# Kernel tuning notes

Measured on AMD Instinct MI355X. Metric: run time of the kernel, lower is better.

The kernel has to match this reference:

```python
import math
import jax, jax.numpy as jnp
import numpy as np

MODEL_DIM = 4096
NUM_EXPERTS = 64
NUM_TOKENS = 8192
CAPACITY_FACTOR = 1.0


def setup_inputs() -> dict:
    key = jax.random.key(0)
    kx, kw = jax.random.split(key)
    x = jax.random.normal(kx, (NUM_TOKENS, MODEL_DIM), dtype=jnp.float32)
    # nn.Linear weight: [num_experts, model_dim]
    W = jax.random.normal(kw, (NUM_EXPERTS, MODEL_DIM), dtype=jnp.float32) * (1.0 / math.sqrt(MODEL_DIM))
    return {"x": x, "W": W}


def reference(x, W):
    # gating projection (no bias), cast to fp32 as in top1gating
    logits = jnp.matmul(x, W.T).astype(jnp.float32)  # [S, E]
    num_tokens, num_experts = logits.shape
    capacity = int(CAPACITY_FACTOR * math.ceil(num_tokens / num_experts))

    indices1_s = jnp.argmax(logits, axis=1)                        # [S]
    gates = jax.nn.softmax(logits, axis=1)                         # [S, E]
    mask1 = jax.nn.one_hot(indices1_s, num_experts, dtype=jnp.float32)  # [S, E]
    gates1_s = jnp.sum(gates * mask1, axis=1)                      # [S]
    # per-expert running position of each routed token
    locations1 = jnp.cumsum(mask1, axis=0) - 1.0                   # [S, E]
    locations1_s = jnp.sum(locations1 * mask1, axis=1)             # [S]

    return (indices1_s.astype(jnp.int32),
            capacity,
            locations1_s.astype(jnp.int32),
            gates1_s,
            num_experts)
```

## Files before the change

kernel.cpp:

```cpp
#include <hip/hip_runtime.h>
#include <math.h>

#define NTOK 8192
#define MDIM 4096
#define NEXP 64
#define CAPACITY 128.0f

#define OFF_IDX  0
#define OFF_CAP  8192
#define OFF_LOC  8193
#define OFF_GATE 16385
#define OFF_NE   24577

#define NSLICE 16
#define KSL    (MDIM / NSLICE)
#define KC     32
#define NCH    (KSL / KC)

#define WS_CNT_OFF  0
#define WS_RK_OFF   16384
#define WS_PART_OFF 24576

using bf16x8 = __attribute__((ext_vector_type(8))) short;
using f32x4  = __attribute__((ext_vector_type(4))) float;
typedef unsigned int u32;

static __device__ __forceinline__ u32 cvtpk(float a0, float a1) {
    u32 r;
    asm("v_cvt_pk_bf16_f32 %0, %1, %2" : "=v"(r) : "v"(a0), "v"(a1));
    return r;
}

static __device__ __forceinline__ void split2(
    float a0, float a1, u32& p1, u32& p2, u32& p3)
{
    p1 = cvtpk(a0, a1);
    float t0 = a0 - __uint_as_float(p1 << 16);
    float t1 = a1 - __uint_as_float(p1 & 0xffff0000u);
    p2 = cvtpk(t0, t1);
    float u0 = t0 - __uint_as_float(p2 << 16);
    float u1 = t1 - __uint_as_float(p2 & 0xffff0000u);
    p3 = cvtpk(u0, u1);
}

__global__ __launch_bounds__(512, 4) void gate_mfma(
    const float* __restrict__ x,
    const float* __restrict__ W,
    float* __restrict__ part)
{
    __shared__ __align__(16) unsigned short wl[12][64][32];

    const int tid   = threadIdx.x;
    const int lane  = tid & 63;
    const int wv    = tid >> 6;
    const int m     = lane & 15;
    const int g     = lane >> 4;
    const int tok0  = blockIdx.x * 256 + wv * 32;
    const int slice = blockIdx.y;
    const int k0    = slice * KSL;

    const float* __restrict__ xp = x + (size_t)(tok0 + m) * MDIM + k0 + g * 8;

    auto loadx = [&](int c, float4* d) {
        const float* p = xp + c * KC;
        d[0] = *(const float4*)(p);
        d[1] = *(const float4*)(p + 4);
        d[2] = *(const float4*)(p + 16 * MDIM);
        d[3] = *(const float4*)(p + 16 * MDIM + 4);
    };

    auto splitW = [&](int h) {
        #pragma unroll
        for (int r = 0; r < 4; ++r) {
            const int j4  = r * 512 + tid;
            const int e   = j4 >> 5;
            const int kk4 = j4 & 31;
            float4 v = *(const float4*)(W + (size_t)e * MDIM + k0 + h * 128 + kk4 * 4);
            const int c4     = kk4 >> 3;
            const int slog   = (kk4 >> 1) & 3;
            const int half16 = kk4 & 1;
            const int phys   = slog ^ ((e >> 1) & 3);
            u32 w1a, w2a, w3a, w1b, w2b, w3b;
            split2(v.x, v.y, w1a, w2a, w3a);
            split2(v.z, v.w, w1b, w2b, w3b);
            *(uint2*)&wl[c4 * 3 + 0][e][phys * 8 + half16 * 4] = make_uint2(w1a, w1b);
            *(uint2*)&wl[c4 * 3 + 1][e][phys * 8 + half16 * 4] = make_uint2(w2a, w2b);
            *(uint2*)&wl[c4 * 3 + 2][e][phys * 8 + half16 * 4] = make_uint2(w3a, w3b);
        }
    };

    auto cvt = [&](float4 lo, float4 hi, bf16x8& r0, bf16x8& r1, bf16x8& r2) {
        union { u32 u[4]; bf16x8 v; } P1, P2, P3;
        split2(lo.x, lo.y, P1.u[0], P2.u[0], P3.u[0]);
        split2(lo.z, lo.w, P1.u[1], P2.u[1], P3.u[1]);
        split2(hi.x, hi.y, P1.u[2], P2.u[2], P3.u[2]);
        split2(hi.z, hi.w, P1.u[3], P2.u[3], P3.u[3]);
        r0 = P1.v; r1 = P2.v; r2 = P3.v;
    };

    f32x4 acc[2][4];
    #pragma unroll
    for (int gr = 0; gr < 2; ++gr)
        #pragma unroll
        for (int nt = 0; nt < 4; ++nt) acc[gr][nt] = (f32x4){0.f, 0.f, 0.f, 0.f};

    float4 bufA[4], bufB[4];
    loadx(0, bufA);
    loadx(1, bufB);

    #pragma unroll
    for (int h = 0; h < 2; ++h) {
        if (h) __syncthreads();
        splitW(h);
        __syncthreads();

        #pragma unroll
        for (int c4 = 0; c4 < 4; ++c4) {
            const int c = h * 4 + c4;
            float4* buf = (c & 1) ? bufB : bufA;

            bf16x8 w[3][4];
            #pragma unroll
            for (int t = 0; t < 3; ++t)
                #pragma unroll
                for (int nt = 0; nt < 4; ++nt) {
                    const int e    = nt * 16 + m;
                    const int phys = g ^ ((e >> 1) & 3);
                    w[t][nt] = *(const bf16x8*)&wl[c4 * 3 + t][e][phys * 8];
                }

            bf16x8 a[2][3];
            cvt(buf[0], buf[1], a[0][0], a[0][1], a[0][2]);
            cvt(buf[2], buf[3], a[1][0], a[1][1], a[1][2]);

            if (c + 2 < NCH) loadx(c + 2, buf);

            #pragma unroll
            for (int gr = 0; gr < 2; ++gr)
                #pragma unroll
                for (int nt = 0; nt < 4; ++nt)
                    acc[gr][nt] = __builtin_amdgcn_mfma_f32_16x16x32_bf16(a[gr][2], w[0][nt], acc[gr][nt], 0, 0, 0);
            #pragma unroll
            for (int gr = 0; gr < 2; ++gr)
                #pragma unroll
                for (int nt = 0; nt < 4; ++nt)
                    acc[gr][nt] = __builtin_amdgcn_mfma_f32_16x16x32_bf16(a[gr][0], w[2][nt], acc[gr][nt], 0, 0, 0);
            #pragma unroll
            for (int gr = 0; gr < 2; ++gr)
                #pragma unroll
                for (int nt = 0; nt < 4; ++nt)
                    acc[gr][nt] = __builtin_amdgcn_mfma_f32_16x16x32_bf16(a[gr][1], w[1][nt], acc[gr][nt], 0, 0, 0);
            #pragma unroll
            for (int gr = 0; gr < 2; ++gr)
                #pragma unroll
                for (int nt = 0; nt < 4; ++nt)
                    acc[gr][nt] = __builtin_amdgcn_mfma_f32_16x16x32_bf16(a[gr][1], w[0][nt], acc[gr][nt], 0, 0, 0);
            #pragma unroll
            for (int gr = 0; gr < 2; ++gr)
                #pragma unroll
                for (int nt = 0; nt < 4; ++nt)
                    acc[gr][nt] = __builtin_amdgcn_mfma_f32_16x16x32_bf16(a[gr][0], w[1][nt], acc[gr][nt], 0, 0, 0);
            #pragma unroll
            for (int gr = 0; gr < 2; ++gr)
                #pragma unroll
                for (int nt = 0; nt < 4; ++nt)
                    acc[gr][nt] = __builtin_amdgcn_mfma_f32_16x16x32_bf16(a[gr][0], w[0][nt], acc[gr][nt], 0, 0, 0);
        }
    }

    #pragma unroll
    for (int gr = 0; gr < 2; ++gr)
        #pragma unroll
        for (int nt = 0; nt < 4; ++nt)
            #pragma unroll
            for (int r = 0; r < 4; ++r) {
                const int tokr = tok0 + gr * 16 + g * 4 + r;
                part[((size_t)slice * NTOK + tokr) * 64 + nt * 16 + m] = acc[gr][nt][r];
            }
}

template<int S>
__global__ __launch_bounds__(256) void reduce_count(
    const float* __restrict__ part,
    float* __restrict__ out,
    int* __restrict__ cnt,
    int* __restrict__ rk)
{
    __shared__ int eidx[32];

    const int tid  = threadIdx.x;
    const int tok0 = blockIdx.x * 32;
    const int trel = tid >> 3;
    const int tok  = tok0 + trel;
    const int q    = tid & 7;

    const float4* __restrict__ p4 = (const float4*)part;

    float4 a[2];
    #pragma unroll
    for (int r = 0; r < 2; ++r) a[r] = make_float4(0.f, 0.f, 0.f, 0.f);
    for (int s = 0; s < S; ++s) {
        #pragma unroll
        for (int r = 0; r < 2; ++r) {
            float4 v = p4[((size_t)s * NTOK + tok) * 16 + q * 2 + r];
            a[r].x += v.x; a[r].y += v.y; a[r].z += v.z; a[r].w += v.w;
        }
    }

    float vals[8] = {a[0].x, a[0].y, a[0].z, a[0].w,
                     a[1].x, a[1].y, a[1].z, a[1].w};

    float bm = vals[0];
    int   be = q * 8;
    #pragma unroll
    for (int j = 1; j < 8; ++j)
        if (vals[j] > bm) { bm = vals[j]; be = q * 8 + j; }
    #pragma unroll
    for (int off = 1; off <= 4; off <<= 1) {
        float om = __shfl_xor(bm, off, 64);
        int   oe = __shfl_xor(be, off, 64);
        if (om > bm || (om == bm && oe < be)) { bm = om; be = oe; }
    }

    float es = 0.f;
    #pragma unroll
    for (int j = 0; j < 8; ++j) es += expf(vals[j] - bm);
    #pragma unroll
    for (int off = 1; off <= 4; off <<= 1)
        es += __shfl_xor(es, off, 64);

    if (q == 0) {
        out[OFF_IDX  + tok] = (float)be;
        out[OFF_GATE + tok] = 1.0f / es;
        eidx[trel] = be;
    }
    __syncthreads();

    if (tid < 64) {
        const int e = (tid < 32) ? eidx[tid] : -1;
        const unsigned long long lt =
            (tid == 0) ? 0ull : ((~0ull) >> (64 - tid));
        unsigned long long mymask = 0;
        int myrk = 0;
        for (int ee = 0; ee < 64; ++ee) {
            unsigned long long mb = __ballot(e == ee);
            if (tid == ee) mymask = mb;
            if (e == ee)   myrk   = (int)__popcll(mb & lt);
        }
        cnt[blockIdx.x * 64 + tid] = (int)__popcll(mymask);
        if (tid < 32) rk[tok0 + tid] = myrk;
    }
    if (tid == 0 && blockIdx.x == 0) {
        out[OFF_CAP] = CAPACITY;
        out[OFF_NE]  = (float)NEXP;
    }
}

__global__ __launch_bounds__(512) void scan_emit(
    const float* __restrict__ idxf,
    const int* __restrict__ cnt,
    const int* __restrict__ rk,
    float* __restrict__ out)
{
    __shared__ int sc[256][64];
    __shared__ int ps[64][8];

    const int tid = threadIdx.x;
    const int e   = tid >> 3;
    const int q   = tid & 7;

    #pragma unroll
    for (int r = 0; r < 32; ++r) sc[0][r * 512 + tid] = cnt[r * 512 + tid];
    __syncthreads();

    {
        int sum = 0;
        #pragma unroll
        for (int j = 0; j < 32; ++j) sum += sc[q * 32 + j][e];
        ps[e][q] = sum;
    }
    __syncthreads();

    {
        int base = 0;
        for (int qq = 0; qq < 8; ++qq) { if (qq < q) base += ps[e][qq]; }
        #pragma unroll
        for (int j = 0; j < 32; ++j) {
            int ch = q * 32 + j;
            int v  = sc[ch][e];
            sc[ch][e] = base;
            base += v;
        }
    }
    __syncthreads();

    #pragma unroll
    for (int r = 0; r < 16; ++r) {
        const int s  = r * 512 + tid;
        const int ee = (int)idxf[s];
        out[OFF_LOC + s] = (float)(sc[s >> 5][ee] + rk[s]);
    }
}

extern "C" void kernel_launch(void* const* d_in, const int* in_sizes, int n_in,
                              void* d_out, int out_size, void* d_ws, size_t ws_size,
                              hipStream_t stream)
{
    const float* x = (const float*)d_in[0];
    const float* W = (const float*)d_in[1];
    float* out = (float*)d_out;

    int*   cnt  = (int*)d_ws + WS_CNT_OFF;
    int*   rk   = (int*)d_ws + WS_RK_OFF;
    float* part = (float*)d_ws + WS_PART_OFF;

    gate_mfma<<<dim3(32, NSLICE), 512, 0, stream>>>(x, W, part);
    reduce_count<NSLICE><<<256, 256, 0, stream>>>(part, out, cnt, rk);
    scan_emit<<<1, 512, 0, stream>>>(out + OFF_IDX, cnt, rk, out);
}
```

Measured before the change: 232.3 us.

## Accumulate split-K partials with atomics and fuse scan into reduction via last-block

Each K-slice of the gating GEMM now adds its partial logits straight into one zeroed logits buffer with float atomics, instead of writing 16 separate partial buffers that a second kernel summed. The reduction kernel reads logits once, and the last block to finish (found with an atomic counter) runs the per-expert prefix scan and writes locations, which removes the third launch. This costs a memset before the GEMM and atomic contention on the output. It also makes the logit sums order-nondeterministic, which could flip argmax ties.

```diff
diff --git a/kernel.cpp b/kernel.cpp
--- a/kernel.cpp
+++ b/kernel.cpp
@@ -19,7 +19,8 @@
 
 #define WS_CNT_OFF  0
 #define WS_RK_OFF   16384
-#define WS_PART_OFF 24576
+#define WS_LG_OFF   24576
+#define WS_DONE_OFF (24576 + 524288)
 
 using bf16x8 = __attribute__((ext_vector_type(8))) short;
 using f32x4  = __attribute__((ext_vector_type(4))) float;
@@ -46,7 +47,7 @@
 __global__ __launch_bounds__(512, 4) void gate_mfma(
     const float* __restrict__ x,
     const float* __restrict__ W,
-    float* __restrict__ part)
+    float* __restrict__ logits)
 {
     __shared__ __align__(16) unsigned short wl[12][64][32];
 
@@ -175,18 +176,22 @@
             #pragma unroll
             for (int r = 0; r < 4; ++r) {
                 const int tokr = tok0 + gr * 16 + g * 4 + r;
-                part[((size_t)slice * NTOK + tokr) * 64 + nt * 16 + m] = acc[gr][nt][r];
+                unsafeAtomicAdd(&logits[(size_t)tokr * 64 + nt * 16 + m],
+                                acc[gr][nt][r]);
             }
 }
 
-template<int S>
-__global__ __launch_bounds__(256) void reduce_count(
-    const float* __restrict__ part,
+__global__ __launch_bounds__(256) void reduce_scan(
+    const float* __restrict__ logits,
     float* __restrict__ out,
     int* __restrict__ cnt,
-    int* __restrict__ rk)
+    int* __restrict__ rk,
+    int* __restrict__ done)
 {
     __shared__ int eidx[32];
+    __shared__ int isLast;
+    __shared__ int sc[256][64];
+    __shared__ int ps[64][4];
 
     const int tid  = threadIdx.x;
     const int tok0 = blockIdx.x * 32;
@@ -194,21 +199,11 @@
     const int tok  = tok0 + trel;
     const int q    = tid & 7;
 
-    const float4* __restrict__ p4 = (const float4*)part;
-
-    float4 a[2];
-    #pragma unroll
-    for (int r = 0; r < 2; ++r) a[r] = make_float4(0.f, 0.f, 0.f, 0.f);
-    for (int s = 0; s < S; ++s) {
-        #pragma unroll
-        for (int r = 0; r < 2; ++r) {
-            float4 v = p4[((size_t)s * NTOK + tok) * 16 + q * 2 + r];
-            a[r].x += v.x; a[r].y += v.y; a[r].z += v.z; a[r].w += v.w;
-        }
-    }
-
-    float vals[8] = {a[0].x, a[0].y, a[0].z, a[0].w,
-                     a[1].x, a[1].y, a[1].z, a[1].w};
+    const float4* __restrict__ p4 = (const float4*)logits;
+
+    float4 a0 = p4[(size_t)tok * 16 + q * 2 + 0];
+    float4 a1 = p4[(size_t)tok * 16 + q * 2 + 1];
+    float vals[8] = {a0.x, a0.y, a0.z, a0.w, a1.x, a1.y, a1.z, a1.w};
 
     float bm = vals[0];
     int   be = q * 8;
@@ -254,49 +249,48 @@
         out[OFF_CAP] = CAPACITY;
         out[OFF_NE]  = (float)NEXP;
     }
-}
-
-__global__ __launch_bounds__(512) void scan_emit(
-    const float* __restrict__ idxf,
-    const int* __restrict__ cnt,
-    const int* __restrict__ rk,
-    float* __restrict__ out)
-{
-    __shared__ int sc[256][64];
-    __shared__ int ps[64][8];
-
-    const int tid = threadIdx.x;
-    const int e   = tid >> 3;
-    const int q   = tid & 7;
-
-    #pragma unroll
-    for (int r = 0; r < 32; ++r) sc[0][r * 512 + tid] = cnt[r * 512 + tid];
+
+    __threadfence();
+    if (tid == 0) {
+        int t = atomicAdd(done, 1);
+        isLast = (t == 255);
+    }
+    __syncthreads();
+    if (!isLast) return;
+
+    const int e = tid & 63;
+    const int s4 = tid >> 6;
+
+    #pragma unroll
+    for (int r = 0; r < 64; ++r)
+        ((int*)sc)[r * 256 + tid] = cnt[r * 256 + tid];
     __syncthreads();
 
     {
         int sum = 0;
         #pragma unroll
-        for (int j = 0; j < 32; ++j) sum += sc[q * 32 + j][e];
-        ps[e][q] = sum;
+        for (int j = 0; j < 64; ++j) sum += sc[s4 * 64 + j][e];
+        ps[e][s4] = sum;
     }
     __syncthreads();
 
     {
         int base = 0;
-        for (int qq = 0; qq < 8; ++qq) { if (qq < q) base += ps[e][qq]; }
-        #pragma unroll
-        for (int j = 0; j < 32; ++j) {
-            int ch = q * 32 + j;
-            int v  = sc[ch][e];
+        for (int qq = 0; qq < 4; ++qq) { if (qq < s4) base += ps[e][qq]; }
+        #pragma unroll
+        for (int j = 0; j < 64; ++j) {
+            const int ch = s4 * 64 + j;
+            const int v  = sc[ch][e];
             sc[ch][e] = base;
             base += v;
         }
     }
     __syncthreads();
 
-    #pragma unroll
-    for (int r = 0; r < 16; ++r) {
-        const int s  = r * 512 + tid;
+    const float* idxf = out + OFF_IDX;
+    #pragma unroll
+    for (int r = 0; r < 32; ++r) {
+        const int s  = r * 256 + tid;
         const int ee = (int)idxf[s];
         out[OFF_LOC + s] = (float)(sc[s >> 5][ee] + rk[s]);
     }
@@ -310,11 +304,13 @@
     const float* W = (const float*)d_in[1];
     float* out = (float*)d_out;
 
-    int*   cnt  = (int*)d_ws + WS_CNT_OFF;
-    int*   rk   = (int*)d_ws + WS_RK_OFF;
-    float* part = (float*)d_ws + WS_PART_OFF;
-
-    gate_mfma<<<dim3(32, NSLICE), 512, 0, stream>>>(x, W, part);
-    reduce_count<NSLICE><<<256, 256, 0, stream>>>(part, out, cnt, rk);
-    scan_emit<<<1, 512, 0, stream>>>(out + OFF_IDX, cnt, rk, out);
-}
+    int*   cnt    = (int*)d_ws + WS_CNT_OFF;
+    int*   rk     = (int*)d_ws + WS_RK_OFF;
+    float* logits = (float*)((int*)d_ws + WS_LG_OFF);
+    int*   done   = (int*)d_ws + WS_DONE_OFF;
+
+    hipMemsetAsync(logits, 0, (size_t)(524288 + 16) * 4, stream);
+
+    gate_mfma<<<dim3(32, NSLICE), 512, 0, stream>>>(x, W, logits);
+    reduce_scan<<<256, 256, 0, stream>>>(logits, out, cnt, rk, done);
+}
```

Result: slower. 243.7 us (+4.9%).
